# Kernel optimization log

Hardware: AMD Instinct MI355X
Metric: run time of the kernel (lower is better)

## Reference

```python
import jax, jax.numpy as jnp
import numpy as np

N_USERS = 100000
N_ITEMS = 50000
EMB_DIM = 64
N_LAYERS = 3
N_EDGES = 4000000
N_NODES = N_USERS + N_ITEMS


def setup_inputs() -> dict:
    key = jax.random.key(0)
    k1, k2, k3 = jax.random.split(key, 3)
    edge_index = jax.random.randint(k1, (2, N_EDGES), 0, N_NODES, dtype=jnp.int64)
    # nn.init.normal_(std=0.1)
    user_w = 0.1 * jax.random.normal(k2, (N_USERS, EMB_DIM), dtype=jnp.float32)
    item_w = 0.1 * jax.random.normal(k3, (N_ITEMS, EMB_DIM), dtype=jnp.float32)
    return {"edge_index": edge_index, "user_w": user_w, "item_w": item_w}


def reference(edge_index, user_w, item_w):
    n_users = user_w.shape[0]
    n_nodes = n_users + item_w.shape[0]
    row, col = edge_index[0], edge_index[1]

    x = jnp.concatenate([user_w, item_w], axis=0)  # [N, d]

    # degree of target nodes (col), with deg^-0.5 and inf -> 0
    deg = jax.ops.segment_sum(jnp.ones(row.shape, x.dtype), col, num_segments=n_nodes)
    deg_inv_sqrt = jnp.where(deg > 0, jax.lax.rsqrt(jnp.where(deg > 0, deg, 1.0)), 0.0)
    norm = deg_inv_sqrt[row] * deg_inv_sqrt[col]  # [E]

    # n_layers of gather-scale-scatter propagation; mean over (n_layers+1) states
    acc = x
    total = x
    for _ in range(N_LAYERS):
        msgs = norm[:, None] * acc[row]  # [E, d]
        acc = jax.ops.segment_sum(msgs, col, num_segments=n_nodes)
        total = total + acc
    final_emb = total / jnp.asarray(N_LAYERS + 1, x.dtype)

    return final_emb[:n_users], final_emb[n_users:]
```

## Files before the change

kernel.cpp:

```cpp
#include <hip/hip_runtime.h>
#include <hip/hip_fp16.h>


#ifndef EMB
#define EMB 64
#endif
#define BSHIFT 7
#define BNODES (1 << BSHIFT)
#define NBMAX 1280
#define CCAP 4800
#define CH 16384
#define STH 1024

typedef unsigned int uint;
typedef unsigned short ushort;

static __device__ __forceinline__ ushort f2h(float f) {
    __half h = __float2half(f);
    return *(ushort*)&h;
}

static __device__ __forceinline__ void acc2h(uint u, float& aL, float& aH) {
    __half2 h = *(__half2*)&u;
    float2 f = __half22float2(h);
    aL += f.x;
    aH += f.y;
}

static __device__ __forceinline__ float2 h2f2(uint u) {
    __half2 h = *(__half2*)&u;
    return __half22float2(h);
}

__global__ void lgcn_setup_kernel(const int* __restrict__ ei,
                                  int* __restrict__ flag,
                                  int* __restrict__ bcount,
                                  int* __restrict__ bcur,
                                  ushort* __restrict__ z0,
                                  ushort* __restrict__ z1,
                                  ushort* __restrict__ z2,
                                  int NB, int n_elems) {
    __shared__ int any_nz;
    int t = threadIdx.x;
    if (t == 0) any_nz = 0;
    __syncthreads();
    if (t < 128 && ei[2 * t + 1] != 0) atomicOr(&any_nz, 1);
    for (int i = t; i < NB; i += 256) { bcount[i] = 0; bcur[i] = 0; }
    if (t < EMB) {
        z0[n_elems + t] = 0;
        z1[n_elems + t] = 0;
        z2[n_elems + t] = 0;
    }
    __syncthreads();
    if (t == 0) *flag = (any_nz == 0) ? 1 : 0;
}

static __device__ __forceinline__ int load_idx(const int* __restrict__ ei,
                                               long long elem, int is64,
                                               int n_nodes) {
    int v = is64 ? ei[elem << 1] : ei[elem];
    return min(max(v, 0), n_nodes - 1);
}

__global__ void __launch_bounds__(STH)
lgcn_bhist2_kernel(const int* __restrict__ ei,
                   const int* __restrict__ flag,
                   int* __restrict__ hist,
                   int n_edges, int n_nodes, int NB, int nblk) {
    __shared__ int lcount[NBMAX];
    int t = threadIdx.x;
    int blk = blockIdx.x;
    int is64 = *flag;
    long long base = (long long)blk * CH;
    for (int i = t; i < NB; i += STH) lcount[i] = 0;
    __syncthreads();
    for (int k = t; k < CH; k += STH) {
        long long e = base + k;
        if (e < n_edges) {
            int c = load_idx(ei, (long long)n_edges + e, is64, n_nodes);
            atomicAdd(&lcount[c >> BSHIFT], 1);
        }
    }
    __syncthreads();
    for (int i = t; i < NB; i += STH)
        hist[(size_t)i * nblk + blk] = lcount[i];
}

__global__ void lgcn_rowsum_kernel(const int* __restrict__ hist,
                                   int* __restrict__ bcount,
                                   int nblk) {
    __shared__ int red[256];
    int b = blockIdx.x;
    int t = threadIdx.x;
    const int* row = hist + (size_t)b * nblk;
    int s = 0;
    for (int j = t; j < nblk; j += 256) s += row[j];
    red[t] = s;
    __syncthreads();
    for (int off = 128; off > 0; off >>= 1) {
        if (t < off) red[t] += red[t + off];
        __syncthreads();
    }
    if (t == 0) bcount[b] = red[0];
}

__global__ void lgcn_bscan_kernel(const int* __restrict__ bcount,
                                  int* __restrict__ bucketBase,
                                  int* __restrict__ offsets,
                                  int NB, int n_nodes) {
    __shared__ int tsum[256];
    int t = threadIdx.x;
    int K = (NB + 255) / 256;
    int base = t * K;
    int s = 0;
    for (int k = 0; k < K; ++k) {
        int i = base + k;
        if (i < NB) s += bcount[i];
    }
    tsum[t] = s;
    __syncthreads();
    for (int off = 1; off < 256; off <<= 1) {
        int x = (t >= off) ? tsum[t - off] : 0;
        __syncthreads();
        tsum[t] += x;
        __syncthreads();
    }
    int run = tsum[t] - s;
    for (int k = 0; k < K; ++k) {
        int i = base + k;
        if (i < NB) { bucketBase[i] = run; run += bcount[i]; }
    }
    if (t == 255) {
        bucketBase[NB] = tsum[255];
        offsets[n_nodes] = tsum[255];
    }
}

__global__ void __launch_bounds__(STH)
lgcn_bscatter3_kernel(const int* __restrict__ ei,
                      const int* __restrict__ flag,
                      const int* __restrict__ bucketBase,
                      int* __restrict__ bcur,
                      uint* __restrict__ pairs,
                      int n_edges, int n_nodes, int NB) {
    __shared__ int lcount[NBMAX];
    __shared__ int lloc[NBMAX];
    __shared__ int ldelta[NBMAX];
    __shared__ int tsum[STH];
    __shared__ int ltot;
    __shared__ uint stage[CH];
    __shared__ ushort stageb[CH];
    int t = threadIdx.x;
    int is64 = *flag;
    long long base = (long long)blockIdx.x * CH;
    for (int i = t; i < NB; i += STH) lcount[i] = 0;
    __syncthreads();
    for (int k = t; k < CH; k += STH) {
        long long e = base + k;
        if (e < n_edges) {
            int c = load_idx(ei, (long long)n_edges + e, is64, n_nodes);
            atomicAdd(&lcount[c >> BSHIFT], 1);
        }
    }
    __syncthreads();
    {
        int K = (NB + STH - 1) / STH;
        int cbase = t * K;
        int s = 0;
        for (int k = 0; k < K; ++k) {
            int i = cbase + k;
            if (i < NB) s += lcount[i];
        }
        tsum[t] = s;
        __syncthreads();
        for (int off = 1; off < STH; off <<= 1) {
            int x = (t >= off) ? tsum[t - off] : 0;
            __syncthreads();
            tsum[t] += x;
            __syncthreads();
        }
        int run = tsum[t] - s;
        for (int k = 0; k < K; ++k) {
            int i = cbase + k;
            if (i < NB) { lloc[i] = run; run += lcount[i]; }
        }
        if (t == STH - 1) ltot = tsum[t];
    }
    __syncthreads();
    for (int i = t; i < NB; i += STH) {
        int cnt = lcount[i];
        ldelta[i] = cnt ? (bucketBase[i] + atomicAdd(&bcur[i], cnt) - lloc[i]) : 0;
        lcount[i] = 0;
    }
    __syncthreads();
    for (int k = t; k < CH; k += STH) {
        long long e = base + k;
        if (e < n_edges) {
            int r = load_idx(ei, e, is64, n_nodes);
            int c = load_idx(ei, (long long)n_edges + e, is64, n_nodes);
            int b = c >> BSHIFT;
            int pos = lloc[b] + atomicAdd(&lcount[b], 1);
            stage[pos] = ((uint)r << BSHIFT) | (uint)(c & (BNODES - 1));
            stageb[pos] = (ushort)b;
        }
    }
    __syncthreads();
    int tot = ltot;
    for (int k = t; k < tot; k += STH) {
        pairs[ldelta[stageb[k]] + k] = stage[k];
    }
}

__global__ void lgcn_bcsr_kernel(const uint* __restrict__ pairs,
                                 const int* __restrict__ bucketBase,
                                 const float* __restrict__ user_w,
                                 const float* __restrict__ item_w,
                                 int* __restrict__ offsets,
                                 int* __restrict__ csr_rows,
                                 float* __restrict__ dis,
                                 ushort* __restrict__ z0,
                                 int n_user_elems, int n_nodes) {
    __shared__ int deg[BNODES];
    __shared__ int tmp[BNODES];
    __shared__ int loffx[BNODES];
    __shared__ int cur[BNODES];
    __shared__ float disL[BNODES];
    __shared__ uint lp[CCAP];
    int b = blockIdx.x;
    int t = threadIdx.x;
    int nodeStart = b << BSHIFT;
    int base = bucketBase[b];
    int span = bucketBase[b + 1] - base;
    bool fits = (span <= CCAP);
    if (t < BNODES) deg[t] = 0;
    __syncthreads();
    for (int i = t; i < span; i += 256) {
        uint p = pairs[base + i];
        if (fits) lp[i] = p;
        atomicAdd(&deg[p & (BNODES - 1)], 1);
    }
    __syncthreads();
    if (t < BNODES) tmp[t] = deg[t];
    __syncthreads();
    for (int off = 1; off < BNODES; off <<= 1) {
        int x = (t < BNODES && t >= off) ? tmp[t - off] : 0;
        __syncthreads();
        if (t < BNODES) tmp[t] += x;
        __syncthreads();
    }
    if (t < BNODES) {
        int excl = tmp[t] - deg[t];
        loffx[t] = excl;
        cur[t] = 0;
        float d = (deg[t] > 0) ? rsqrtf((float)deg[t]) : 0.0f;
        disL[t] = d;
        int node = nodeStart + t;
        if (node < n_nodes) {
            offsets[node] = base + excl;
            dis[node] = d;
        }
    }
    __syncthreads();
    for (int i = t; i < span; i += 256) {
        uint p = fits ? lp[i] : pairs[base + i];
        int cl = (int)(p & (BNODES - 1));
        int pos = loffx[cl] + atomicAdd(&cur[cl], 1);
        csr_rows[base + pos] = (int)(p >> BSHIFT);
    }
    int eBase = nodeStart << 6;
    for (int e4 = t; e4 < (BNODES << 4); e4 += 256) {
        int e = e4 << 2;
        int node = nodeStart + (e >> 6);
        if (node < n_nodes) {
            int gi = eBase + e;
            float4 v = (gi < n_user_elems)
                ? *(const float4*)(user_w + gi)
                : *(const float4*)(item_w + (gi - n_user_elems));
            float d = disL[e >> 6];
            ushort4 o;
            o.x = f2h(d * v.x); o.y = f2h(d * v.y);
            o.z = f2h(d * v.z); o.w = f2h(d * v.w);
            *(ushort4*)(z0 + gi) = o;
        }
    }
}

template <bool FUSE>
__global__ void lgcn_gather_kernel(const int* __restrict__ csr_rows,
                                   const int* __restrict__ offsets,
                                   const float* __restrict__ dis,
                                   const ushort* __restrict__ zin,
                                   ushort* __restrict__ zout,
                                   const ushort* __restrict__ zprev,
                                   const float* __restrict__ user_w,
                                   const float* __restrict__ item_w,
                                   float* __restrict__ out,
                                   int n_user_elems, int n_nodes) {
    long long tid = (long long)blockIdx.x * blockDim.x + threadIdx.x;
    int c    = (int)(tid >> 6);
    int lane = threadIdx.x & 63;
    int oct  = lane >> 3;
    int o8   = lane & 7;
    if (c >= n_nodes) return;
    int beg = offsets[c];
    int end = offsets[c + 1];
    int deg = end - beg;
    float a[8];
    #pragma unroll
    for (int k = 0; k < 8; ++k) a[k] = 0.0f;

    if (deg > 0) {
        int n1 = deg < 64 ? deg : 64;
        int ng = (n1 + 7) >> 3;
        int rr[8];
        #pragma unroll
        for (int g = 0; g < 8; ++g) {
            int s = g * 8 + oct;
            if (g < ng) {
                int r = csr_rows[beg + (s < n1 ? s : 0)];
                rr[g] = (s < n1) ? r : n_nodes;
            } else {
                rr[g] = n_nodes;
            }
        }
        uint4 q[8];
        #pragma unroll
        for (int g = 0; g < 8; ++g)
            if (g < ng)
                q[g] = *(const uint4*)(zin + (size_t)rr[g] * EMB + o8 * 8);
        #pragma unroll
        for (int g = 0; g < 8; ++g) {
            if (g < ng) {
                acc2h(q[g].x, a[0], a[1]);
                acc2h(q[g].y, a[2], a[3]);
                acc2h(q[g].z, a[4], a[5]);
                acc2h(q[g].w, a[6], a[7]);
            }
        }
        for (int j = beg + 64; j < end; j += 16) {
            int j0 = j + oct;
            int j1 = j + 8 + oct;
            bool v0 = j0 < end;
            bool v1 = j1 < end;
            int r0 = csr_rows[v0 ? j0 : beg]; r0 = v0 ? r0 : n_nodes;
            int r1 = csr_rows[v1 ? j1 : beg]; r1 = v1 ? r1 : n_nodes;
            uint4 q0 = *(const uint4*)(zin + (size_t)r0 * EMB + o8 * 8);
            uint4 q1 = *(const uint4*)(zin + (size_t)r1 * EMB + o8 * 8);
            acc2h(q0.x, a[0], a[1]);
            acc2h(q0.y, a[2], a[3]);
            acc2h(q0.z, a[4], a[5]);
            acc2h(q0.w, a[6], a[7]);
            acc2h(q1.x, a[0], a[1]);
            acc2h(q1.y, a[2], a[3]);
            acc2h(q1.z, a[4], a[5]);
            acc2h(q1.w, a[6], a[7]);
        }
    }

    #pragma unroll
    for (int k = 0; k < 8; ++k) {
        a[k] += __shfl_xor(a[k], 8, 64);
        a[k] += __shfl_xor(a[k], 16, 64);
        a[k] += __shfl_xor(a[k], 32, 64);
    }

    if (oct == 0) {
        float dc = dis[c];
        size_t fo = (size_t)c * EMB + o8 * 8;
        if (!FUSE) {
            float s2 = dc * dc;
            uint4 v;
            v.x = ((uint)f2h(s2 * a[1]) << 16) | f2h(s2 * a[0]);
            v.y = ((uint)f2h(s2 * a[3]) << 16) | f2h(s2 * a[2]);
            v.z = ((uint)f2h(s2 * a[5]) << 16) | f2h(s2 * a[4]);
            v.w = ((uint)f2h(s2 * a[7]) << 16) | f2h(s2 * a[6]);
            *(uint4*)(zout + fo) = v;
        } else {
            float inv = (dc > 0.0f) ? 1.0f / dc : 0.0f;
            uint4 v1 = *(const uint4*)(zprev + fo);
            uint4 v2 = *(const uint4*)(zin + fo);
            float4 x0, x1;
            if ((int)fo < n_user_elems) {
                x0 = *(const float4*)(user_w + fo);
                x1 = *(const float4*)(user_w + fo + 4);
            } else {
                size_t j = fo - n_user_elems;
                x0 = *(const float4*)(item_w + j);
                x1 = *(const float4*)(item_w + j + 4);
            }
            float2 p, q;
            float4 o0, o1;
            p = h2f2(v1.x); q = h2f2(v2.x);
            o0.x = 0.25f * (x0.x + inv * (p.x + q.x) + dc * a[0]);
            o0.y = 0.25f * (x0.y + inv * (p.y + q.y) + dc * a[1]);
            p = h2f2(v1.y); q = h2f2(v2.y);
            o0.z = 0.25f * (x0.z + inv * (p.x + q.x) + dc * a[2]);
            o0.w = 0.25f * (x0.w + inv * (p.y + q.y) + dc * a[3]);
            p = h2f2(v1.z); q = h2f2(v2.z);
            o1.x = 0.25f * (x1.x + inv * (p.x + q.x) + dc * a[4]);
            o1.y = 0.25f * (x1.y + inv * (p.y + q.y) + dc * a[5]);
            p = h2f2(v1.w); q = h2f2(v2.w);
            o1.z = 0.25f * (x1.z + inv * (p.x + q.x) + dc * a[6]);
            o1.w = 0.25f * (x1.w + inv * (p.y + q.y) + dc * a[7]);
            *(float4*)(out + fo) = o0;
            *(float4*)(out + fo + 4) = o1;
        }
    }
}

extern "C" void kernel_launch(void* const* d_in, const int* in_sizes, int n_in,
                              void* d_out, int out_size, void* d_ws, size_t ws_size,
                              hipStream_t stream) {
    int ie = 0, iu = 1, ii = 2;
    {
        long long s[3] = { in_sizes[0], in_sizes[1], in_sizes[2] };
        ie = 0;
        if (s[1] > s[ie]) ie = 1;
        if (s[2] > s[ie]) ie = 2;
        int rest[2], k = 0;
        for (int j = 0; j < 3; ++j) if (j != ie) rest[k++] = j;
        if (s[rest[0]] >= s[rest[1]]) { iu = rest[0]; ii = rest[1]; }
        else                          { iu = rest[1]; ii = rest[0]; }
    }
    const int*   edge_index = (const int*)d_in[ie];
    const float* user_w     = (const float*)d_in[iu];
    const float* item_w     = (const float*)d_in[ii];
    float* out = (float*)d_out;

    const int n_edges = in_sizes[ie] / 2;
    const int n_users = in_sizes[iu] / EMB;
    const int n_items = in_sizes[ii] / EMB;
    const int n_nodes = n_users + n_items;
    const int n_elems = n_nodes * EMB;
    const int NB = (n_nodes + BNODES - 1) / BNODES;
    const int nblk = (n_edges + CH - 1) / CH;

    auto align_up = [](size_t x) { return (x + 1023) & ~(size_t)1023; };
    char* w = (char*)d_ws;
    int*   flag       = (int*)w; w += 1024;
    int*   bcount     = (int*)w; w += align_up((size_t)NB * sizeof(int));
    int*   bucketBase = (int*)w; w += align_up(((size_t)NB + 1) * sizeof(int));
    int*   bcur       = (int*)w; w += align_up((size_t)NB * sizeof(int));
    int*   offsets    = (int*)w; w += align_up(((size_t)n_nodes + 1) * sizeof(int));
    float* dis        = (float*)w; w += align_up((size_t)n_nodes * sizeof(float));
    int*   csr_rows   = (int*)w; w += align_up((size_t)n_edges * sizeof(int));
    size_t u_bytes = align_up(((size_t)n_elems + EMB) * sizeof(ushort));
    size_t p_bytes = align_up((size_t)n_edges * sizeof(uint));
    size_t slot0   = (u_bytes > p_bytes ? u_bytes : p_bytes);
    size_t h_bytes = align_up((size_t)NB * nblk * sizeof(int));
    char*  slot0p = w;
    uint*  pairs  = (uint*)slot0p; w += slot0;
    ushort* z0    = (ushort*)w; w += u_bytes;
    ushort* z1    = (ushort*)w; w += u_bytes;
    ushort* z2    = (ushort*)w; w += u_bytes;
    int* hist;
    if (slot0 >= p_bytes + h_bytes) {
        hist = (int*)(slot0p + p_bytes);
    } else {
        hist = (int*)w; w += h_bytes;
    }

    lgcn_setup_kernel<<<1, 256, 0, stream>>>(edge_index, flag, bcount, bcur,
                                             z0, z1, z2, NB, n_elems);

    lgcn_bhist2_kernel<<<nblk, STH, 0, stream>>>(
        edge_index, flag, hist, n_edges, n_nodes, NB, nblk);
    lgcn_rowsum_kernel<<<NB, 256, 0, stream>>>(hist, bcount, nblk);
    lgcn_bscan_kernel<<<1, 256, 0, stream>>>(bcount, bucketBase, offsets, NB, n_nodes);
    lgcn_bscatter3_kernel<<<nblk, STH, 0, stream>>>(
        edge_index, flag, bucketBase, bcur, pairs, n_edges, n_nodes, NB);
    lgcn_bcsr_kernel<<<NB, 256, 0, stream>>>(
        pairs, bucketBase, user_w, item_w, offsets, csr_rows, dis, z0,
        n_users * EMB, n_nodes);

    {
        const int BLK = 256;
        long long n_thr = (long long)n_nodes * 64;
        int gW = (int)((n_thr + BLK - 1) / BLK);
        lgcn_gather_kernel<false><<<gW, BLK, 0, stream>>>(
            csr_rows, offsets, dis, z0, z1,
            nullptr, nullptr, nullptr, nullptr, 0, n_nodes);
        lgcn_gather_kernel<false><<<gW, BLK, 0, stream>>>(
            csr_rows, offsets, dis, z1, z2,
            nullptr, nullptr, nullptr, nullptr, 0, n_nodes);
        lgcn_gather_kernel<true><<<gW, BLK, 0, stream>>>(
            csr_rows, offsets, dis, z2, nullptr,
            z1, user_w, item_w, out, n_users * EMB, n_nodes);
    }
}
```

Before: 417.3 us.

## Replace scatter-side recount and global atomics with per-block histogram prefix scan

The row-sum kernel becomes a per-bucket exclusive scan over block histograms, producing a run base for every (bucket, block) pair. The scatter kernel then reads its counts from the stored histogram instead of re-reading column indices and re-counting with shared atomics. It also computes destination offsets directly instead of doing a global atomicAdd on a bucket cursor, which removes the bcur zeroing. In exchange it needs an extra histogram-sized buffer, and the scan assumes nblk is at most 256. The bucket order also becomes deterministic.

```diff
diff --git a/kernel.cpp b/kernel.cpp
--- a/kernel.cpp
+++ b/kernel.cpp
@@ -34,18 +34,15 @@
 
 __global__ void lgcn_setup_kernel(const int* __restrict__ ei,
                                   int* __restrict__ flag,
-                                  int* __restrict__ bcount,
-                                  int* __restrict__ bcur,
                                   ushort* __restrict__ z0,
                                   ushort* __restrict__ z1,
                                   ushort* __restrict__ z2,
-                                  int NB, int n_elems) {
+                                  int n_elems) {
     __shared__ int any_nz;
     int t = threadIdx.x;
     if (t == 0) any_nz = 0;
     __syncthreads();
     if (t < 128 && ei[2 * t + 1] != 0) atomicOr(&any_nz, 1);
-    for (int i = t; i < NB; i += 256) { bcount[i] = 0; bcur[i] = 0; }
     if (t < EMB) {
         z0[n_elems + t] = 0;
         z1[n_elems + t] = 0;
@@ -86,22 +83,26 @@
         hist[(size_t)i * nblk + blk] = lcount[i];
 }
 
-__global__ void lgcn_rowsum_kernel(const int* __restrict__ hist,
-                                   int* __restrict__ bcount,
-                                   int nblk) {
-    __shared__ int red[256];
+__global__ void lgcn_rowscan_kernel(const int* __restrict__ hist,
+                                    int* __restrict__ runbase,
+                                    int* __restrict__ bcount,
+                                    int nblk) {
+    __shared__ int tsum[256];
     int b = blockIdx.x;
     int t = threadIdx.x;
     const int* row = hist + (size_t)b * nblk;
-    int s = 0;
-    for (int j = t; j < nblk; j += 256) s += row[j];
-    red[t] = s;
-    __syncthreads();
-    for (int off = 128; off > 0; off >>= 1) {
-        if (t < off) red[t] += red[t + off];
-        __syncthreads();
-    }
-    if (t == 0) bcount[b] = red[0];
+    int* orow = runbase + (size_t)b * nblk;
+    int v = (t < nblk) ? row[t] : 0;
+    tsum[t] = v;
+    __syncthreads();
+    for (int off = 1; off < 256; off <<= 1) {
+        int x = (t >= off) ? tsum[t - off] : 0;
+        __syncthreads();
+        tsum[t] += x;
+        __syncthreads();
+    }
+    if (t < nblk) orow[t] = tsum[t] - v;
+    if (t == 255) bcount[b] = tsum[255];
 }
 
 __global__ void lgcn_bscan_kernel(const int* __restrict__ bcount,
@@ -137,12 +138,13 @@
 }
 
 __global__ void __launch_bounds__(STH)
-lgcn_bscatter3_kernel(const int* __restrict__ ei,
+lgcn_bscatter4_kernel(const int* __restrict__ ei,
                       const int* __restrict__ flag,
                       const int* __restrict__ bucketBase,
-                      int* __restrict__ bcur,
+                      const int* __restrict__ hist,
+                      const int* __restrict__ runbase,
                       uint* __restrict__ pairs,
-                      int n_edges, int n_nodes, int NB) {
+                      int n_edges, int n_nodes, int NB, int nblk) {
     __shared__ int lcount[NBMAX];
     __shared__ int lloc[NBMAX];
     __shared__ int ldelta[NBMAX];
@@ -151,17 +153,11 @@
     __shared__ uint stage[CH];
     __shared__ ushort stageb[CH];
     int t = threadIdx.x;
+    int blk = blockIdx.x;
     int is64 = *flag;
-    long long base = (long long)blockIdx.x * CH;
-    for (int i = t; i < NB; i += STH) lcount[i] = 0;
-    __syncthreads();
-    for (int k = t; k < CH; k += STH) {
-        long long e = base + k;
-        if (e < n_edges) {
-            int c = load_idx(ei, (long long)n_edges + e, is64, n_nodes);
-            atomicAdd(&lcount[c >> BSHIFT], 1);
-        }
-    }
+    long long base = (long long)blk * CH;
+    for (int i = t; i < NB; i += STH)
+        lcount[i] = hist[(size_t)i * nblk + blk];
     __syncthreads();
     {
         int K = (NB + STH - 1) / STH;
@@ -188,8 +184,7 @@
     }
     __syncthreads();
     for (int i = t; i < NB; i += STH) {
-        int cnt = lcount[i];
-        ldelta[i] = cnt ? (bucketBase[i] + atomicAdd(&bcur[i], cnt) - lloc[i]) : 0;
+        ldelta[i] = bucketBase[i] + runbase[(size_t)i * nblk + blk] - lloc[i];
         lcount[i] = 0;
     }
     __syncthreads();
@@ -440,7 +435,6 @@
     int*   flag       = (int*)w; w += 1024;
     int*   bcount     = (int*)w; w += align_up((size_t)NB * sizeof(int));
     int*   bucketBase = (int*)w; w += align_up(((size_t)NB + 1) * sizeof(int));
-    int*   bcur       = (int*)w; w += align_up((size_t)NB * sizeof(int));
     int*   offsets    = (int*)w; w += align_up(((size_t)n_nodes + 1) * sizeof(int));
     float* dis        = (float*)w; w += align_up((size_t)n_nodes * sizeof(float));
     int*   csr_rows   = (int*)w; w += align_up((size_t)n_edges * sizeof(int));
@@ -453,22 +447,25 @@
     ushort* z0    = (ushort*)w; w += u_bytes;
     ushort* z1    = (ushort*)w; w += u_bytes;
     ushort* z2    = (ushort*)w; w += u_bytes;
-    int* hist;
-    if (slot0 >= p_bytes + h_bytes) {
-        hist = (int*)(slot0p + p_bytes);
+    int* hist; int* runbase;
+    if (slot0 >= p_bytes + 2 * h_bytes) {
+        hist    = (int*)(slot0p + p_bytes);
+        runbase = (int*)(slot0p + p_bytes + h_bytes);
     } else {
-        hist = (int*)w; w += h_bytes;
-    }
-
-    lgcn_setup_kernel<<<1, 256, 0, stream>>>(edge_index, flag, bcount, bcur,
-                                             z0, z1, z2, NB, n_elems);
+        hist    = (int*)w; w += h_bytes;
+        runbase = (int*)w; w += h_bytes;
+    }
+
+    lgcn_setup_kernel<<<1, 256, 0, stream>>>(edge_index, flag, z0, z1, z2,
+                                             n_elems);
 
     lgcn_bhist2_kernel<<<nblk, STH, 0, stream>>>(
         edge_index, flag, hist, n_edges, n_nodes, NB, nblk);
-    lgcn_rowsum_kernel<<<NB, 256, 0, stream>>>(hist, bcount, nblk);
+    lgcn_rowscan_kernel<<<NB, 256, 0, stream>>>(hist, runbase, bcount, nblk);
     lgcn_bscan_kernel<<<1, 256, 0, stream>>>(bcount, bucketBase, offsets, NB, n_nodes);
-    lgcn_bscatter3_kernel<<<nblk, STH, 0, stream>>>(
-        edge_index, flag, bucketBase, bcur, pairs, n_edges, n_nodes, NB);
+    lgcn_bscatter4_kernel<<<nblk, STH, 0, stream>>>(
+        edge_index, flag, bucketBase, hist, runbase, pairs,
+        n_edges, n_nodes, NB, nblk);
     lgcn_bcsr_kernel<<<NB, 256, 0, stream>>>(
         pairs, bucketBase, user_w, item_w, offsets, csr_rows, dis, z0,
         n_users * EMB, n_nodes);
```

Result: faster. 407.9 us (-2.3%).
